# Kernel optimization log

Hardware: AMD Instinct MI355X
Metric: run time of the kernel (lower is better)

Reference implementation:

```python
import jax, jax.numpy as jnp
import numpy as np

B, S, D, H = 4, 2048, 1024, 4096  # batch, seq, d_model, mlp hidden
EPS = 1e-12  # F.normalize eps


def _linear(x, W, b):
    return x @ W.T + b


def setup_inputs() -> dict:
    key = jax.random.key(0)
    ks = jax.random.split(key, 14)
    s = lambda d: 1.0 / np.sqrt(d)
    return {
        "x": jax.random.normal(ks[0], (B, S, D), dtype=jnp.float32),
        "Wq": jax.random.normal(ks[1], (D, D), dtype=jnp.float32) * s(D),
        "bq": jax.random.normal(ks[2], (D,), dtype=jnp.float32) * 0.01,
        "Wk": jax.random.normal(ks[3], (D, D), dtype=jnp.float32) * s(D),
        "bk": jax.random.normal(ks[4], (D,), dtype=jnp.float32) * 0.01,
        "Wv": jax.random.normal(ks[5], (D, D), dtype=jnp.float32) * s(D),
        "bv": jax.random.normal(ks[6], (D,), dtype=jnp.float32) * 0.01,
        "W1": jax.random.normal(ks[7], (D, D), dtype=jnp.float32) * s(D),
        "b1": jax.random.normal(ks[8], (D,), dtype=jnp.float32) * 0.01,
        "W2": jax.random.normal(ks[9], (H, D), dtype=jnp.float32) * s(D),
        "b2": jax.random.normal(ks[10], (H,), dtype=jnp.float32) * 0.01,
        "W3": jax.random.normal(ks[11], (D, H), dtype=jnp.float32) * s(H),
        "b3": jax.random.normal(ks[12], (D,), dtype=jnp.float32) * 0.01,
    }


def reference(x, Wq, bq, Wk, bk, Wv, bv, W1, b1, W2, b2, W3, b3):
    Q = _linear(x, Wq, bq)  # [B,S,D]
    K = _linear(x, Wk, bk)
    V = _linear(x, Wv, bv)
    # L2-normalize along feature dim (F.normalize, p=2, dim=2)
    Q = Q / jnp.maximum(jnp.linalg.norm(Q, axis=2, keepdims=True), EPS)
    K = K / jnp.maximum(jnp.linalg.norm(K, axis=2, keepdims=True), EPS)
    sim = jnp.einsum("bqd,bkd->bqk", Q, K)  # cosine similarities [B,S,S]
    attn = jax.nn.softmax(sim, axis=2)
    out = jnp.einsum("bqk,bkd->bqd", attn, V)  # [B,S,D]
    # MLP: Linear->relu->Linear->relu->Linear (dropout identity in eval)
    h = jax.nn.relu(_linear(out, W1, b1))
    h = jax.nn.relu(_linear(h, W2, b2))
    return _linear(h, W3, b3)
```

## Files before the change

kernel.cpp:

```cpp
#include <hip/hip_runtime.h>


using u16 = unsigned short;
using bf16x8 = __attribute__((ext_vector_type(8))) __bf16;
using f32x4  = __attribute__((ext_vector_type(4))) float;

__device__ __forceinline__ u16 f2bf(float f) {
  unsigned u = __float_as_uint(f);
  unsigned r = (u + 0x7FFFu + ((u >> 16) & 1u)) >> 16;
  return (u16)r;
}
__device__ __forceinline__ float bf2f(u16 h) {
  return __uint_as_float(((unsigned)h) << 16);
}

struct CastSegs {
  const float* src[7];
  u16* dst[7];
  long beg[8];
};
__global__ __launch_bounds__(256) void cast_multi_kernel(CastSegs cs) {
  long idx = (long)blockIdx.x * 256 + threadIdx.x;
  if (idx >= cs.beg[7]) return;
  int seg = 0;
#pragma unroll
  for (int s = 1; s < 7; ++s) seg += (idx >= cs.beg[s]) ? 1 : 0;
  const long loc = idx - cs.beg[seg];
  float4 v = reinterpret_cast<const float4*>(cs.src[seg])[loc];
  ushort4 o;
  o.x = f2bf(v.x); o.y = f2bf(v.y); o.z = f2bf(v.z); o.w = f2bf(v.w);
  reinterpret_cast<ushort4*>(cs.dst[seg])[loc] = o;
}

__global__ __launch_bounds__(256) void l2norm_kernel(
    const u16* __restrict__ in, u16* __restrict__ out) {
  __shared__ float red[4];
  long row = blockIdx.x;
  const int tid = threadIdx.x, lane = tid & 63, wave = tid >> 6;
  ushort4 h = *reinterpret_cast<const ushort4*>(in + row * 1024 + tid * 4);
  float x0 = bf2f(h.x), x1 = bf2f(h.y), x2 = bf2f(h.z), x3 = bf2f(h.w);
  float ss = x0 * x0 + x1 * x1 + x2 * x2 + x3 * x3;
#pragma unroll
  for (int o = 32; o; o >>= 1) ss += __shfl_xor(ss, o);
  if (lane == 0) red[wave] = ss;
  __syncthreads();
  ss = red[0] + red[1] + red[2] + red[3];
  float s = 1.0f / fmaxf(sqrtf(ss), 1e-12f);
  ushort4 o;
  o.x = f2bf(x0 * s); o.y = f2bf(x1 * s); o.z = f2bf(x2 * s); o.w = f2bf(x3 * s);
  *reinterpret_cast<ushort4*>(out + row * 1024 + tid * 4) = o;
}

__global__ void transpose_kernel(const u16* __restrict__ in, u16* __restrict__ out,
                                 int rows, int cols) {
  __shared__ u16 t[32][33];
  const int c0 = blockIdx.x * 32, r0 = blockIdx.y * 32;
  const long off = (long)blockIdx.z * rows * cols;
  const u16* ib = in + off;
  u16* ob = out + off;
  const int tx = threadIdx.x, ty = threadIdx.y;
#pragma unroll
  for (int j = 0; j < 4; ++j)
    t[ty + j * 8][tx] = ib[(long)(r0 + ty + j * 8) * cols + c0 + tx];
  __syncthreads();
#pragma unroll
  for (int j = 0; j < 4; ++j)
    ob[(long)(c0 + ty + j * 8) * rows + r0 + tx] = t[tx][ty + j * 8];
}

__global__ __launch_bounds__(256) void softmax_kernel(
    const float* __restrict__ in, u16* __restrict__ out) {
  __shared__ float red[4];
  long row = blockIdx.x;
  const int tid = threadIdx.x, lane = tid & 63, wave = tid >> 6;
  const float* p = in + row * 2048;
  float v[8];
  float4 a = *reinterpret_cast<const float4*>(p + tid * 8);
  float4 b = *reinterpret_cast<const float4*>(p + tid * 8 + 4);
  v[0] = a.x; v[1] = a.y; v[2] = a.z; v[3] = a.w;
  v[4] = b.x; v[5] = b.y; v[6] = b.z; v[7] = b.w;
  float m = v[0];
#pragma unroll
  for (int i = 1; i < 8; ++i) m = fmaxf(m, v[i]);
#pragma unroll
  for (int o = 32; o; o >>= 1) m = fmaxf(m, __shfl_xor(m, o));
  if (lane == 0) red[wave] = m;
  __syncthreads();
  m = fmaxf(fmaxf(red[0], red[1]), fmaxf(red[2], red[3]));
  float s = 0.0f;
#pragma unroll
  for (int i = 0; i < 8; ++i) { v[i] = __expf(v[i] - m); s += v[i]; }
#pragma unroll
  for (int o = 32; o; o >>= 1) s += __shfl_xor(s, o);
  __syncthreads();
  if (lane == 0) red[wave] = s;
  __syncthreads();
  s = red[0] + red[1] + red[2] + red[3];
  float inv = 1.0f / s;
  ushort4 o0, o1;
  o0.x = f2bf(v[0] * inv); o0.y = f2bf(v[1] * inv);
  o0.z = f2bf(v[2] * inv); o0.w = f2bf(v[3] * inv);
  o1.x = f2bf(v[4] * inv); o1.y = f2bf(v[5] * inv);
  o1.z = f2bf(v[6] * inv); o1.w = f2bf(v[7] * inv);
  *reinterpret_cast<ushort4*>(out + row * 2048 + tid * 8) = o0;
  *reinterpret_cast<ushort4*>(out + row * 2048 + tid * 8 + 4) = o1;
}

template <int BM, int DEPTH, int MODE>
__global__ __launch_bounds__(512, 2) void gemm8p(
    const u16* __restrict__ A, const u16* __restrict__ Bw,
    const float* __restrict__ bias, void* __restrict__ Cout,
    const float* __restrict__ bias2, void* __restrict__ Cout2,
    const float* __restrict__ bias3, void* __restrict__ Cout3,
    int N, int K, long batchA, long batchB, long batchC, int relu,
    int gx, int gy) {
  constexpr int MF  = BM / 32;
  constexpr int MH  = MF / 2;
  constexpr int ASZ = BM * 64;
  constexpr int BSZ = 256 * 64;
  constexpr int AR  = BM / 64;
  __shared__ u16 lds[DEPTH * (ASZ + BSZ)];
  u16* const ldsA = lds;
  u16* const ldsB = lds + DEPTH * ASZ;

  const int nwg = gridDim.x;
  const int lid = blockIdx.x;
  const int q = nwg >> 3, r = nwg & 7;
  const int xcd = lid & 7, jj = lid >> 3;
  const int wg = (xcd < r ? xcd * (q + 1) : r * (q + 1) + (xcd - r) * q) + jj;
  const int bx = wg % gx;
  const int rest = wg / gx;
  const int by = rest % gy;
  const int bz = rest / gy;

  const int tid = threadIdx.x, wave = tid >> 6, lane = tid & 63;
  const int wr = wave >> 2, wc = wave & 3;
  const int fr = lane & 15, hi = lane >> 4;

  const long Abase = bz * batchA + (long)by * BM * K;
  const long Bbase = bz * batchB + (long)bx * 256 * K;

  int aoff[MF][2], boff[4][2];
#pragma unroll
  for (int m = 0; m < MF; ++m) {
    const int qm = m / MH, ml = m % MH;
    const int row = qm * (BM / 2) + wr * (BM / 4) + ml * 16 + fr;
#pragma unroll
    for (int ks = 0; ks < 2; ++ks) {
      const int gg = ks * 4 + hi;
      aoff[m][ks] = row * 64 + ((gg ^ (row & 7)) * 8);
    }
  }
#pragma unroll
  for (int n = 0; n < 4; ++n) {
    const int qn = n >> 1, nl = n & 1;
    const int row = qn * 128 + wc * 32 + nl * 16 + fr;
#pragma unroll
    for (int ks = 0; ks < 2; ++ks) {
      const int gg = ks * 4 + hi;
      boff[n][ks] = row * 64 + ((gg ^ (row & 7)) * 8);
    }
  }

  const int rA = wave * 8 + (lane >> 3);
  const int g8 = (((lane & 7) ^ (lane >> 3)) * 8);
  long asrc[AR], bsrc[4];
#pragma unroll
  for (int rr = 0; rr < AR; ++rr) asrc[rr] = Abase + (long)(rr * 64 + rA) * K + g8;
#pragma unroll
  for (int rr = 0; rr < 4; ++rr) bsrc[rr] = Bbase + (long)(rr * 64 + rA) * K + g8;

#define STAGE_A(bufp, rr, k0)                                                  \
  __builtin_amdgcn_global_load_lds(                                            \
      (const __attribute__((address_space(1))) void*)(A + asrc[rr] + (k0)),    \
      (__attribute__((address_space(3))) void*)((bufp) + (rr) * 4096 + wave * 512), \
      16, 0, 0)
#define STAGE_B(bufp, rr, k0)                                                  \
  __builtin_amdgcn_global_load_lds(                                            \
      (const __attribute__((address_space(1))) void*)(Bw + bsrc[rr] + (k0)),   \
      (__attribute__((address_space(3))) void*)((bufp) + (rr) * 4096 + wave * 512), \
      16, 0, 0)

  const int NT = K >> 6;

  if constexpr (DEPTH == 2) {
#pragma unroll
    for (int rr = 0; rr < AR; ++rr) STAGE_A(ldsA, rr, 0);
#pragma unroll
    for (int rr = 0; rr < 4; ++rr) STAGE_B(ldsB, rr, 0);
    asm volatile("s_waitcnt vmcnt(0)" ::: "memory");
  } else {
#pragma unroll
    for (int rr = 0; rr < AR; ++rr) STAGE_A(ldsA, rr, 0);
#pragma unroll
    for (int rr = 0; rr < 4; ++rr) STAGE_B(ldsB, rr, 0);
    if (NT > 1) {
#pragma unroll
      for (int rr = 0; rr < AR; ++rr) STAGE_A(ldsA + ASZ, rr, 64);
#pragma unroll
      for (int rr = 0; rr < 4; ++rr) STAGE_B(ldsB + BSZ, rr, 64);
      asm volatile("s_waitcnt vmcnt(6)" ::: "memory");
    } else {
      asm volatile("s_waitcnt vmcnt(0)" ::: "memory");
    }
  }
  __builtin_amdgcn_s_barrier();

  f32x4 acc[MF][4] = {};

#define READ_AHALF(dst, h)                                                     \
  _Pragma("unroll") for (int mm = 0; mm < MH; ++mm)                            \
  _Pragma("unroll") for (int ks = 0; ks < 2; ++ks)                             \
    dst[mm][ks] = *reinterpret_cast<const bf16x8*>(&curA[aoff[(h) * MH + mm][ks]]);
#define READ_BHALF(dst, h)                                                     \
  _Pragma("unroll") for (int nn = 0; nn < 2; ++nn)                             \
  _Pragma("unroll") for (int ks = 0; ks < 2; ++ks)                             \
    dst[nn][ks] = *reinterpret_cast<const bf16x8*>(&curB[boff[(h) * 2 + nn][ks]]);
#define MFMA_Q(ah, bh, qm, qn)                                                 \
  __builtin_amdgcn_s_setprio(1);                                               \
  _Pragma("unroll") for (int ks = 0; ks < 2; ++ks)                             \
  _Pragma("unroll") for (int mm = 0; mm < MH; ++mm)                            \
  _Pragma("unroll") for (int nn = 0; nn < 2; ++nn)                             \
    acc[(qm) * MH + mm][(qn) * 2 + nn] =                                       \
        __builtin_amdgcn_mfma_f32_16x16x32_bf16(                               \
            ah[mm][ks], bh[nn][ks], acc[(qm) * MH + mm][(qn) * 2 + nn], 0, 0, 0); \
  __builtin_amdgcn_s_setprio(0);

  for (int t = 0; t < NT; ++t) {
    u16* curA = ldsA + (t % DEPTH) * ASZ;
    u16* curB = ldsB + (t % DEPTH) * BSZ;
    const int ts = t + DEPTH - 1;
    const bool st = ts < NT;
    u16* nxtA = ldsA + (ts % DEPTH) * ASZ;
    u16* nxtB = ldsB + (ts % DEPTH) * BSZ;
    const int k0n = ts << 6;

    bf16x8 a0[MH][2], a1[MH][2], b0[2][2], b1[2][2];

    READ_AHALF(a0, 0)
    READ_BHALF(b0, 0)
    if (st) {
#pragma unroll
      for (int rr = 0; rr < AR / 2; ++rr) STAGE_A(nxtA, rr, k0n);
    }
    __builtin_amdgcn_s_barrier();
    MFMA_Q(a0, b0, 0, 0)
    if constexpr (DEPTH == 2) {
      if (st) asm volatile("s_waitcnt vmcnt(2)" ::: "memory");
      else    asm volatile("s_waitcnt vmcnt(0)" ::: "memory");
    }
    __builtin_amdgcn_s_barrier();

    READ_BHALF(b1, 1)
    if (st) {
#pragma unroll
      for (int rr = AR / 2; rr < AR; ++rr) STAGE_A(nxtA, rr, k0n);
    }
    __builtin_amdgcn_s_barrier();
    MFMA_Q(a0, b1, 0, 1)
    __builtin_amdgcn_s_barrier();

    READ_AHALF(a1, 1)
    if (st) { STAGE_B(nxtB, 0, k0n); STAGE_B(nxtB, 1, k0n); }
    __builtin_amdgcn_s_barrier();
    MFMA_Q(a1, b0, 1, 0)
    __builtin_amdgcn_s_barrier();

    if (st) { STAGE_B(nxtB, 2, k0n); STAGE_B(nxtB, 3, k0n); }
    __builtin_amdgcn_s_barrier();
    MFMA_Q(a1, b1, 1, 1)
    if constexpr (DEPTH == 2) {
      if (st) asm volatile("s_waitcnt vmcnt(2)" ::: "memory");
    } else {
      if (st) asm volatile("s_waitcnt vmcnt(6)" ::: "memory");
      else    asm volatile("s_waitcnt vmcnt(0)" ::: "memory");
    }
    __builtin_amdgcn_s_barrier();
  }
#undef STAGE_A
#undef STAGE_B
#undef READ_AHALF
#undef READ_BHALF
#undef MFMA_Q

  const long cbase = bz * batchC;
  const int crow = by * BM;
  int ccol = bx * 256;
  const float* bp = bias;
  void* cp = Cout;
  bool obf = (MODE == 1) || (MODE == 2);
  int Nst = N;
  if constexpr (MODE == 2) {
    const int sel = ccol >> 10;
    if (sel == 1) { bp = bias2; cp = Cout2; }
    else if (sel == 2) { bp = bias3; cp = Cout3; }
    ccol &= 1023;
    Nst = 1024;
  }
#pragma unroll
  for (int m = 0; m < MF; ++m) {
    const int qm = m / MH, ml = m % MH;
    const int r0 = crow + qm * (BM / 2) + wr * (BM / 4) + ml * 16 + hi * 4;
#pragma unroll
    for (int n = 0; n < 4; ++n) {
      const int qn = n >> 1, nl = n & 1;
      const int c = ccol + qn * 128 + wc * 32 + nl * 16 + fr;
      const float bb = bp ? bp[c] : 0.0f;
#pragma unroll
      for (int j = 0; j < 4; ++j) {
        float v = acc[m][n][j] + bb;
        if (relu) v = fmaxf(v, 0.0f);
        const long idx = cbase + (long)(r0 + j) * Nst + c;
        if (obf) ((u16*)cp)[idx] = f2bf(v);
        else     ((float*)cp)[idx] = v;
      }
    }
  }
}

extern "C" void kernel_launch(void* const* d_in, const int* in_sizes, int n_in,
                              void* d_out, int out_size, void* d_ws, size_t ws_size,
                              hipStream_t stream) {
  (void)in_sizes; (void)n_in; (void)out_size; (void)ws_size;
  const float* x  = (const float*)d_in[0];
  const float* Wq = (const float*)d_in[1];
  const float* bq = (const float*)d_in[2];
  const float* Wk = (const float*)d_in[3];
  const float* bk = (const float*)d_in[4];
  const float* Wv = (const float*)d_in[5];
  const float* bv = (const float*)d_in[6];
  const float* W1 = (const float*)d_in[7];
  const float* b1 = (const float*)d_in[8];
  const float* W2 = (const float*)d_in[9];
  const float* b2 = (const float*)d_in[10];
  const float* W3 = (const float*)d_in[11];
  const float* b3 = (const float*)d_in[12];

  char* ws = (char*)d_ws;
  const size_t MB = 1u << 20;
  u16* Qbf  = (u16*)(ws + 0);
  u16* Kbf  = Qbf + 8388608;
  float* simf = (float*)(ws + 0);
  u16*   h2   = (u16*)(ws + 0);
  u16* xbf = (u16*)(ws + 64 * MB);
  u16* Vbf = xbf + (size_t)8192 * 1024;
  u16* P   = (u16*)(ws + 64 * MB);
  u16* Wq_b = (u16*)(ws + 96 * MB);
  u16* Wk_b = Wq_b + 1048576;
  u16* Wv_b = Wk_b + 1048576;
  u16* W1_b = Wv_b + 1048576;
  u16* W2_b = W1_b + 1048576;
  u16* W3_b = W2_b + 4194304;
  u16* Qn = (u16*)(ws + 120 * MB);
  u16* Kn = Qn + 8388608;
  u16* Vt = Kn + 8388608;
  u16* attnout = Qn;
  u16* h1      = Kn;

  CastSegs cs;
  cs.src[0] = x;  cs.dst[0] = xbf;
  cs.src[1] = Wq; cs.dst[1] = Wq_b;
  cs.src[2] = Wk; cs.dst[2] = Wk_b;
  cs.src[3] = Wv; cs.dst[3] = Wv_b;
  cs.src[4] = W1; cs.dst[4] = W1_b;
  cs.src[5] = W2; cs.dst[5] = W2_b;
  cs.src[6] = W3; cs.dst[6] = W3_b;
  long szs[7] = {2097152, 262144, 262144, 262144, 262144, 1048576, 1048576};
  long acc0 = 0;
  for (int i = 0; i < 7; ++i) { cs.beg[i] = acc0; acc0 += szs[i]; }
  cs.beg[7] = acc0;
  cast_multi_kernel<<<dim3((unsigned)((acc0 + 255) / 256)), 256, 0, stream>>>(cs);

  gemm8p<128, 3, 2><<<dim3(12 * 64), 512, 0, stream>>>(
      xbf, Wq_b, bq, Qbf, bk, Kbf, bv, Vbf, 3072, 1024, 0, 0, 0, 0, 12, 64);
  l2norm_kernel<<<8192, 256, 0, stream>>>(Qbf, Qn);
  l2norm_kernel<<<8192, 256, 0, stream>>>(Kbf, Kn);
  transpose_kernel<<<dim3(32, 64, 4), dim3(32, 8), 0, stream>>>(Vbf, Vt, 2048, 1024);
  gemm8p<256, 2, 0><<<dim3(8 * 8 * 4), 512, 0, stream>>>(
      Qn, Kn, nullptr, simf, nullptr, nullptr, nullptr, nullptr,
      2048, 1024, 2097152L, 2097152L, 4194304L, 0, 8, 8);
  softmax_kernel<<<8192, 256, 0, stream>>>(simf, P);
  gemm8p<128, 3, 1><<<dim3(4 * 16 * 4), 512, 0, stream>>>(
      P, Vt, nullptr, attnout, nullptr, nullptr, nullptr, nullptr,
      1024, 2048, 4194304L, 2097152L, 2097152L, 0, 4, 16);
  gemm8p<128, 3, 1><<<dim3(4 * 64), 512, 0, stream>>>(
      attnout, W1_b, b1, h1, nullptr, nullptr, nullptr, nullptr,
      1024, 1024, 0, 0, 0, 1, 4, 64);
  gemm8p<256, 2, 1><<<dim3(16 * 32), 512, 0, stream>>>(
      h1, W2_b, b2, h2, nullptr, nullptr, nullptr, nullptr,
      4096, 1024, 0, 0, 0, 1, 16, 32);
  gemm8p<128, 3, 0><<<dim3(4 * 64), 512, 0, stream>>>(
      h2, W3_b, b3, (float*)d_out, nullptr, nullptr, nullptr, nullptr,
      1024, 4096, 0, 0, 0, 0, 4, 64);
}
```

Before: 393.4 us.

## Replace GEMM with register-double-buffered pipeline, bf16 sim scores, fuse l2norms

The GEMM kernel becomes a single 128x256 tile variant. It reads the whole next tile's LDS fragments into a second register set while the MFMAs on the current set run, and uses fewer barriers per k-step. The QK^T similarity GEMM now writes bf16 straight into P, and softmax runs in place from bf16, which halves the traffic of the sim matrix. The two l2norm launches are merged into one. The risks are extra register pressure from holding two fragment sets, precision loss from rounding the logits to bf16 before softmax, and different tile shapes for the former BM=256 GEMMs.

Measured after the change: 392.9 us. No clear change (-0.1%).

```diff
diff --git a/kernel.cpp b/kernel.cpp
--- a/kernel.cpp
+++ b/kernel.cpp
@@ -32,12 +32,17 @@
   reinterpret_cast<ushort4*>(cs.dst[seg])[loc] = o;
 }
 
-__global__ __launch_bounds__(256) void l2norm_kernel(
-    const u16* __restrict__ in, u16* __restrict__ out) {
+__global__ __launch_bounds__(256) void l2norm2_kernel(
+    const u16* __restrict__ Qi, const u16* __restrict__ Ki,
+    u16* __restrict__ Qo, u16* __restrict__ Ko) {
   __shared__ float red[4];
   long row = blockIdx.x;
+  const u16* in;
+  u16* out;
+  if (row < 8192) { in = Qi + row * 1024; out = Qo + row * 1024; }
+  else            { in = Ki + (row - 8192) * 1024; out = Ko + (row - 8192) * 1024; }
   const int tid = threadIdx.x, lane = tid & 63, wave = tid >> 6;
-  ushort4 h = *reinterpret_cast<const ushort4*>(in + row * 1024 + tid * 4);
+  ushort4 h = *reinterpret_cast<const ushort4*>(in + tid * 4);
   float x0 = bf2f(h.x), x1 = bf2f(h.y), x2 = bf2f(h.z), x3 = bf2f(h.w);
   float ss = x0 * x0 + x1 * x1 + x2 * x2 + x3 * x3;
 #pragma unroll
@@ -48,7 +53,7 @@
   float s = 1.0f / fmaxf(sqrtf(ss), 1e-12f);
   ushort4 o;
   o.x = f2bf(x0 * s); o.y = f2bf(x1 * s); o.z = f2bf(x2 * s); o.w = f2bf(x3 * s);
-  *reinterpret_cast<ushort4*>(out + row * 1024 + tid * 4) = o;
+  *reinterpret_cast<ushort4*>(out + tid * 4) = o;
 }
 
 __global__ void transpose_kernel(const u16* __restrict__ in, u16* __restrict__ out,
@@ -69,16 +74,16 @@
 }
 
 __global__ __launch_bounds__(256) void softmax_kernel(
-    const float* __restrict__ in, u16* __restrict__ out) {
+    const u16* __restrict__ in, u16* __restrict__ out) {
   __shared__ float red[4];
   long row = blockIdx.x;
   const int tid = threadIdx.x, lane = tid & 63, wave = tid >> 6;
-  const float* p = in + row * 2048;
+  const u16* p = in + row * 2048 + tid * 8;
+  ushort4 h0 = *reinterpret_cast<const ushort4*>(p);
+  ushort4 h1 = *reinterpret_cast<const ushort4*>(p + 4);
   float v[8];
-  float4 a = *reinterpret_cast<const float4*>(p + tid * 8);
-  float4 b = *reinterpret_cast<const float4*>(p + tid * 8 + 4);
-  v[0] = a.x; v[1] = a.y; v[2] = a.z; v[3] = a.w;
-  v[4] = b.x; v[5] = b.y; v[6] = b.z; v[7] = b.w;
+  v[0] = bf2f(h0.x); v[1] = bf2f(h0.y); v[2] = bf2f(h0.z); v[3] = bf2f(h0.w);
+  v[4] = bf2f(h1.x); v[5] = bf2f(h1.y); v[6] = bf2f(h1.z); v[7] = bf2f(h1.w);
   float m = v[0];
 #pragma unroll
   for (int i = 1; i < 8; ++i) m = fmaxf(m, v[i]);
@@ -106,22 +111,21 @@
   *reinterpret_cast<ushort4*>(out + row * 2048 + tid * 8 + 4) = o1;
 }
 
-template <int BM, int DEPTH, int MODE>
-__global__ __launch_bounds__(512, 2) void gemm8p(
+struct Frags { bf16x8 a[4][2]; bf16x8 b[4][2]; };
+
+template <int MODE>
+__global__ __launch_bounds__(512, 2) void gemmra(
     const u16* __restrict__ A, const u16* __restrict__ Bw,
     const float* __restrict__ bias, void* __restrict__ Cout,
     const float* __restrict__ bias2, void* __restrict__ Cout2,
     const float* __restrict__ bias3, void* __restrict__ Cout3,
     int N, int K, long batchA, long batchB, long batchC, int relu,
     int gx, int gy) {
-  constexpr int MF  = BM / 32;
-  constexpr int MH  = MF / 2;
-  constexpr int ASZ = BM * 64;
+  constexpr int ASZ = 128 * 64;
   constexpr int BSZ = 256 * 64;
-  constexpr int AR  = BM / 64;
-  __shared__ u16 lds[DEPTH * (ASZ + BSZ)];
+  __shared__ u16 lds[2 * (ASZ + BSZ)];
   u16* const ldsA = lds;
-  u16* const ldsB = lds + DEPTH * ASZ;
+  u16* const ldsB = lds + 2 * ASZ;
 
   const int nwg = gridDim.x;
   const int lid = blockIdx.x;
@@ -137,14 +141,14 @@
   const int wr = wave >> 2, wc = wave & 3;
   const int fr = lane & 15, hi = lane >> 4;
 
-  const long Abase = bz * batchA + (long)by * BM * K;
+  const long Abase = bz * batchA + (long)by * 128 * K;
   const long Bbase = bz * batchB + (long)bx * 256 * K;
 
-  int aoff[MF][2], boff[4][2];
-#pragma unroll
-  for (int m = 0; m < MF; ++m) {
-    const int qm = m / MH, ml = m % MH;
-    const int row = qm * (BM / 2) + wr * (BM / 4) + ml * 16 + fr;
+  int aoff[4][2], boff[4][2];
+#pragma unroll
+  for (int m = 0; m < 4; ++m) {
+    const int qm = m >> 1, ml = m & 1;
+    const int row = qm * 64 + wr * 32 + ml * 16 + fr;
 #pragma unroll
     for (int ks = 0; ks < 2; ++ks) {
       const int gg = ks * 4 + hi;
@@ -164,9 +168,9 @@
 
   const int rA = wave * 8 + (lane >> 3);
   const int g8 = (((lane & 7) ^ (lane >> 3)) * 8);
-  long asrc[AR], bsrc[4];
-#pragma unroll
-  for (int rr = 0; rr < AR; ++rr) asrc[rr] = Abase + (long)(rr * 64 + rA) * K + g8;
+  long asrc[2], bsrc[4];
+#pragma unroll
+  for (int rr = 0; rr < 2; ++rr) asrc[rr] = Abase + (long)(rr * 64 + rA) * K + g8;
 #pragma unroll
   for (int rr = 0; rr < 4; ++rr) bsrc[rr] = Bbase + (long)(rr * 64 + rA) * K + g8;
 
@@ -180,115 +184,75 @@
       (const __attribute__((address_space(1))) void*)(Bw + bsrc[rr] + (k0)),   \
       (__attribute__((address_space(3))) void*)((bufp) + (rr) * 4096 + wave * 512), \
       16, 0, 0)
+#define STAGE_TILE(T)                                                          \
+  {                                                                            \
+    u16* sA_ = ldsA + ((T) & 1) * ASZ;                                         \
+    u16* sB_ = ldsB + ((T) & 1) * BSZ;                                         \
+    const int k0_ = (T) << 6;                                                  \
+    STAGE_A(sA_, 0, k0_); STAGE_A(sA_, 1, k0_);                                \
+    STAGE_B(sB_, 0, k0_); STAGE_B(sB_, 1, k0_);                                \
+    STAGE_B(sB_, 2, k0_); STAGE_B(sB_, 3, k0_);                                \
+  }
+#define READ_FRAGS(F, T)                                                       \
+  {                                                                            \
+    u16* rA_ = ldsA + ((T) & 1) * ASZ;                                         \
+    u16* rB_ = ldsB + ((T) & 1) * BSZ;                                         \
+    _Pragma("unroll") for (int m = 0; m < 4; ++m)                              \
+    _Pragma("unroll") for (int ks = 0; ks < 2; ++ks)                           \
+      F.a[m][ks] = *reinterpret_cast<const bf16x8*>(&rA_[aoff[m][ks]]);        \
+    _Pragma("unroll") for (int n = 0; n < 4; ++n)                              \
+    _Pragma("unroll") for (int ks = 0; ks < 2; ++ks)                           \
+      F.b[n][ks] = *reinterpret_cast<const bf16x8*>(&rB_[boff[n][ks]]);        \
+  }
+#define RA_ITER(T, FC, FN)                                                     \
+  {                                                                            \
+    if ((T) + 2 < NT) STAGE_TILE((T) + 2)                                      \
+    if ((T) + 1 < NT) {                                                        \
+      if ((T) + 2 < NT) asm volatile("s_waitcnt vmcnt(6)" ::: "memory");       \
+      else              asm volatile("s_waitcnt vmcnt(0)" ::: "memory");       \
+      __builtin_amdgcn_s_barrier();                                            \
+      READ_FRAGS(FN, (T) + 1)                                                  \
+      __builtin_amdgcn_s_barrier();                                            \
+    }                                                                          \
+    __builtin_amdgcn_s_setprio(1);                                             \
+    _Pragma("unroll") for (int ks = 0; ks < 2; ++ks)                           \
+    _Pragma("unroll") for (int m = 0; m < 4; ++m)                              \
+    _Pragma("unroll") for (int n = 0; n < 4; ++n)                              \
+      acc[m][n] = __builtin_amdgcn_mfma_f32_16x16x32_bf16(                     \
+          FC.a[m][ks], FC.b[n][ks], acc[m][n], 0, 0, 0);                       \
+    __builtin_amdgcn_s_setprio(0);                                             \
+  }
 
   const int NT = K >> 6;
 
-  if constexpr (DEPTH == 2) {
-#pragma unroll
-    for (int rr = 0; rr < AR; ++rr) STAGE_A(ldsA, rr, 0);
-#pragma unroll
-    for (int rr = 0; rr < 4; ++rr) STAGE_B(ldsB, rr, 0);
-    asm volatile("s_waitcnt vmcnt(0)" ::: "memory");
-  } else {
-#pragma unroll
-    for (int rr = 0; rr < AR; ++rr) STAGE_A(ldsA, rr, 0);
-#pragma unroll
-    for (int rr = 0; rr < 4; ++rr) STAGE_B(ldsB, rr, 0);
-    if (NT > 1) {
-#pragma unroll
-      for (int rr = 0; rr < AR; ++rr) STAGE_A(ldsA + ASZ, rr, 64);
-#pragma unroll
-      for (int rr = 0; rr < 4; ++rr) STAGE_B(ldsB + BSZ, rr, 64);
-      asm volatile("s_waitcnt vmcnt(6)" ::: "memory");
-    } else {
-      asm volatile("s_waitcnt vmcnt(0)" ::: "memory");
-    }
-  }
+  f32x4 acc[4][4] = {};
+  Frags fA, fB;
+
+  STAGE_TILE(0)
+  STAGE_TILE(1)
+  asm volatile("s_waitcnt vmcnt(6)" ::: "memory");
   __builtin_amdgcn_s_barrier();
-
-  f32x4 acc[MF][4] = {};
-
-#define READ_AHALF(dst, h)                                                     \
-  _Pragma("unroll") for (int mm = 0; mm < MH; ++mm)                            \
-  _Pragma("unroll") for (int ks = 0; ks < 2; ++ks)                             \
-    dst[mm][ks] = *reinterpret_cast<const bf16x8*>(&curA[aoff[(h) * MH + mm][ks]]);
-#define READ_BHALF(dst, h)                                                     \
-  _Pragma("unroll") for (int nn = 0; nn < 2; ++nn)                             \
-  _Pragma("unroll") for (int ks = 0; ks < 2; ++ks)                             \
-    dst[nn][ks] = *reinterpret_cast<const bf16x8*>(&curB[boff[(h) * 2 + nn][ks]]);
-#define MFMA_Q(ah, bh, qm, qn)                                                 \
-  __builtin_amdgcn_s_setprio(1);                                               \
-  _Pragma("unroll") for (int ks = 0; ks < 2; ++ks)                             \
-  _Pragma("unroll") for (int mm = 0; mm < MH; ++mm)                            \
-  _Pragma("unroll") for (int nn = 0; nn < 2; ++nn)                             \
-    acc[(qm) * MH + mm][(qn) * 2 + nn] =                                       \
-        __builtin_amdgcn_mfma_f32_16x16x32_bf16(                               \
-            ah[mm][ks], bh[nn][ks], acc[(qm) * MH + mm][(qn) * 2 + nn], 0, 0, 0); \
-  __builtin_amdgcn_s_setprio(0);
-
-  for (int t = 0; t < NT; ++t) {
-    u16* curA = ldsA + (t % DEPTH) * ASZ;
-    u16* curB = ldsB + (t % DEPTH) * BSZ;
-    const int ts = t + DEPTH - 1;
-    const bool st = ts < NT;
-    u16* nxtA = ldsA + (ts % DEPTH) * ASZ;
-    u16* nxtB = ldsB + (ts % DEPTH) * BSZ;
-    const int k0n = ts << 6;
-
-    bf16x8 a0[MH][2], a1[MH][2], b0[2][2], b1[2][2];
-
-    READ_AHALF(a0, 0)
-    READ_BHALF(b0, 0)
-    if (st) {
-#pragma unroll
-      for (int rr = 0; rr < AR / 2; ++rr) STAGE_A(nxtA, rr, k0n);
-    }
-    __builtin_amdgcn_s_barrier();
-    MFMA_Q(a0, b0, 0, 0)
-    if constexpr (DEPTH == 2) {
-      if (st) asm volatile("s_waitcnt vmcnt(2)" ::: "memory");
-      else    asm volatile("s_waitcnt vmcnt(0)" ::: "memory");
-    }
-    __builtin_amdgcn_s_barrier();
-
-    READ_BHALF(b1, 1)
-    if (st) {
-#pragma unroll
-      for (int rr = AR / 2; rr < AR; ++rr) STAGE_A(nxtA, rr, k0n);
-    }
-    __builtin_amdgcn_s_barrier();
-    MFMA_Q(a0, b1, 0, 1)
-    __builtin_amdgcn_s_barrier();
-
-    READ_AHALF(a1, 1)
-    if (st) { STAGE_B(nxtB, 0, k0n); STAGE_B(nxtB, 1, k0n); }
-    __builtin_amdgcn_s_barrier();
-    MFMA_Q(a1, b0, 1, 0)
-    __builtin_amdgcn_s_barrier();
-
-    if (st) { STAGE_B(nxtB, 2, k0n); STAGE_B(nxtB, 3, k0n); }
-    __builtin_amdgcn_s_barrier();
-    MFMA_Q(a1, b1, 1, 1)
-    if constexpr (DEPTH == 2) {
-      if (st) asm volatile("s_waitcnt vmcnt(2)" ::: "memory");
-    } else {
-      if (st) asm volatile("s_waitcnt vmcnt(6)" ::: "memory");
-      else    asm volatile("s_waitcnt vmcnt(0)" ::: "memory");
-    }
-    __builtin_amdgcn_s_barrier();
+  READ_FRAGS(fA, 0)
+  asm volatile("s_waitcnt lgkmcnt(0)" ::: "memory");
+  __builtin_amdgcn_sched_barrier(0);
+  __builtin_amdgcn_s_barrier();
+
+  for (int t = 0; t < NT; t += 2) {
+    RA_ITER(t, fA, fB)
+    RA_ITER(t + 1, fB, fA)
   }
 #undef STAGE_A
 #undef STAGE_B
-#undef READ_AHALF
-#undef READ_BHALF
-#undef MFMA_Q
+#undef STAGE_TILE
+#undef READ_FRAGS
+#undef RA_ITER
 
   const long cbase = bz * batchC;
-  const int crow = by * BM;
+  const int crow = by * 128;
   int ccol = bx * 256;
   const float* bp = bias;
   void* cp = Cout;
-  bool obf = (MODE == 1) || (MODE == 2);
+  constexpr bool obf = (MODE == 1) || (MODE == 2);
   int Nst = N;
   if constexpr (MODE == 2) {
     const int sel = ccol >> 10;
@@ -298,9 +262,9 @@
     Nst = 1024;
   }
 #pragma unroll
-  for (int m = 0; m < MF; ++m) {
-    const int qm = m / MH, ml = m % MH;
-    const int r0 = crow + qm * (BM / 2) + wr * (BM / 4) + ml * 16 + hi * 4;
+  for (int m = 0; m < 4; ++m) {
+    const int qm = m >> 1, ml = m & 1;
+    const int r0 = crow + qm * 64 + wr * 32 + ml * 16 + hi * 4;
 #pragma unroll
     for (int n = 0; n < 4; ++n) {
       const int qn = n >> 1, nl = n & 1;
@@ -340,8 +304,7 @@
   const size_t MB = 1u << 20;
   u16* Qbf  = (u16*)(ws + 0);
   u16* Kbf  = Qbf + 8388608;
-  float* simf = (float*)(ws + 0);
-  u16*   h2   = (u16*)(ws + 0);
+  u16* h2   = (u16*)(ws + 0);
   u16* xbf = (u16*)(ws + 64 * MB);
   u16* Vbf = xbf + (size_t)8192 * 1024;
   u16* P   = (u16*)(ws + 64 * MB);
@@ -371,25 +334,24 @@
   cs.beg[7] = acc0;
   cast_multi_kernel<<<dim3((unsigned)((acc0 + 255) / 256)), 256, 0, stream>>>(cs);
 
-  gemm8p<128, 3, 2><<<dim3(12 * 64), 512, 0, stream>>>(
+  gemmra<2><<<dim3(12 * 64), 512, 0, stream>>>(
       xbf, Wq_b, bq, Qbf, bk, Kbf, bv, Vbf, 3072, 1024, 0, 0, 0, 0, 12, 64);
-  l2norm_kernel<<<8192, 256, 0, stream>>>(Qbf, Qn);
-  l2norm_kernel<<<8192, 256, 0, stream>>>(Kbf, Kn);
+  l2norm2_kernel<<<16384, 256, 0, stream>>>(Qbf, Kbf, Qn, Kn);
   transpose_kernel<<<dim3(32, 64, 4), dim3(32, 8), 0, stream>>>(Vbf, Vt, 2048, 1024);
-  gemm8p<256, 2, 0><<<dim3(8 * 8 * 4), 512, 0, stream>>>(
-      Qn, Kn, nullptr, simf, nullptr, nullptr, nullptr, nullptr,
-      2048, 1024, 2097152L, 2097152L, 4194304L, 0, 8, 8);
-  softmax_kernel<<<8192, 256, 0, stream>>>(simf, P);
-  gemm8p<128, 3, 1><<<dim3(4 * 16 * 4), 512, 0, stream>>>(
+  gemmra<1><<<dim3(8 * 16 * 4), 512, 0, stream>>>(
+      Qn, Kn, nullptr, P, nullptr, nullptr, nullptr, nullptr,
+      2048, 1024, 2097152L, 2097152L, 4194304L, 0, 8, 16);
+  softmax_kernel<<<8192, 256, 0, stream>>>(P, P);
+  gemmra<1><<<dim3(4 * 16 * 4), 512, 0, stream>>>(
       P, Vt, nullptr, attnout, nullptr, nullptr, nullptr, nullptr,
       1024, 2048, 4194304L, 2097152L, 2097152L, 0, 4, 16);
-  gemm8p<128, 3, 1><<<dim3(4 * 64), 512, 0, stream>>>(
+  gemmra<1><<<dim3(4 * 64), 512, 0, stream>>>(
       attnout, W1_b, b1, h1, nullptr, nullptr, nullptr, nullptr,
       1024, 1024, 0, 0, 0, 1, 4, 64);
-  gemm8p<256, 2, 1><<<dim3(16 * 32), 512, 0, stream>>>(
+  gemmra<1><<<dim3(16 * 64), 512, 0, stream>>>(
       h1, W2_b, b2, h2, nullptr, nullptr, nullptr, nullptr,
-      4096, 1024, 0, 0, 0, 1, 16, 32);
-  gemm8p<128, 3, 0><<<dim3(4 * 64), 512, 0, stream>>>(
+      4096, 1024, 0, 0, 0, 1, 16, 64);
+  gemmra<0><<<dim3(4 * 64), 512, 0, stream>>>(
       h2, W3_b, b3, (float*)d_out, nullptr, nullptr, nullptr, nullptr,
       1024, 4096, 0, 0, 0, 0, 4, 64);
 }
```
